# Kernel tuning notes

Hardware: AMD Instinct MI355X
Metric: run time of the kernel (lower is better)

The kernel has to match this reference:

```python
import jax, jax.numpy as jnp
import numpy as np

D_MODEL = 1024
NUM_HEADS = 16
HEAD_DIM = D_MODEL // NUM_HEADS


def setup_inputs() -> dict:
    key = jax.random.key(0)
    ks = jax.random.split(key, 9)
    s = 1.0 / np.sqrt(D_MODEL)
    def lin(k):
        kw, kb = jax.random.split(k)
        W = jax.random.uniform(kw, (D_MODEL, D_MODEL), jnp.float32, -s, s)
        b = jax.random.uniform(kb, (D_MODEL,), jnp.float32, -s, s)
        return W, b
    Wq, bq = lin(ks[0])
    Wk, bk = lin(ks[1])
    Wv, bv = lin(ks[2])
    Wo, bo = lin(ks[3])
    x = jax.random.normal(ks[4], (4, 2048, D_MODEL), jnp.float32)
    return {"x": x, "Wq": Wq, "bq": bq, "Wk": Wk, "bk": bk,
            "Wv": Wv, "bv": bv, "Wo": Wo, "bo": bo}


def reference(x, Wq, bq, Wk, bk, Wv, bv, Wo, bo):
    B, S, _ = x.shape
    def heads(W, b):
        # [B,S,D] -> [B,H,S,Dh]
        return (x @ W.T + b).reshape(B, S, NUM_HEADS, HEAD_DIM).transpose(0, 2, 1, 3)
    q = heads(Wq, bq)
    k = heads(Wk, bk)
    v = heads(Wv, bv)
    scale = jnp.sqrt(jnp.float32(HEAD_DIM))
    scores = jnp.einsum('bhqd,bhkd->bhqk', q, k) / scale  # [B,H,S,S]
    attn = jax.nn.softmax(scores, axis=-1)
    ctx = jnp.einsum('bhqk,bhkd->bhqd', attn, v)
    ctx = ctx.transpose(0, 2, 1, 3).reshape(B, S, D_MODEL)
    out = ctx @ Wo.T + bo
    return out
```

## Files before the change

kernel.cpp:

```cpp
#include <hip/hip_runtime.h>
#include <hip/hip_bf16.h>

typedef __bf16 bf16;
typedef __attribute__((ext_vector_type(4))) __bf16 bf16x4;
typedef __attribute__((ext_vector_type(8))) __bf16 bf16x8;
typedef __attribute__((ext_vector_type(4))) float floatx4;

#define MFMA_16x16x32(a, b, c) __builtin_amdgcn_mfma_f32_16x16x32_bf16((a), (b), (c), 0, 0, 0)

__device__ __forceinline__ void async_lds16(const bf16* g, bf16* lds) {
  __builtin_amdgcn_global_load_lds(
      (__attribute__((address_space(1))) void*)(g),
      (__attribute__((address_space(3))) void*)(lds),
      16, 0, 0);
}

__global__ __launch_bounds__(256) void cast_kernel(const float* __restrict__ src,
                                                   bf16* __restrict__ dst, int n) {
  int i = (blockIdx.x * 256 + threadIdx.x) * 8;
  if (i >= n) return;
  floatx4 a = *(const floatx4*)(src + i);
  floatx4 b = *(const floatx4*)(src + i + 4);
  bf16x8 r;
  r[0] = (bf16)a[0]; r[1] = (bf16)a[1]; r[2] = (bf16)a[2]; r[3] = (bf16)a[3];
  r[4] = (bf16)b[0]; r[5] = (bf16)b[1]; r[6] = (bf16)b[2]; r[7] = (bf16)b[3];
  *(bf16x8*)(dst + i) = r;
}

template <typename CT, bool VT>
__device__ __forceinline__ void gemm_async_body(
    const bf16* __restrict__ A, const bf16* __restrict__ W,
    const float* __restrict__ bias, CT* __restrict__ C)
{
  __shared__ __align__(16) bf16 As[128 * 64];
  __shared__ __align__(16) bf16 Bs[128 * 64];

  const int tid  = threadIdx.x;
  const int lane = tid & 63;
  const int wave = tid >> 6;
  const int quad = lane >> 4;
  const int l15  = lane & 15;

  const int gm0   = blockIdx.y * 128;
  const int gn0   = blockIdx.x * 128;
  const int m_off = (wave >> 1) * 64;
  const int n_off = (wave & 1) * 64;

  floatx4 acc[4][4] = {};

  const bf16* ap[4];
  const bf16* wp[4];
  #pragma unroll
  for (int i = 0; i < 4; ++i) {
    int c = i * 256 + tid;
    int srow = c >> 3;
    int ksw  = (c & 7) ^ (srow & 7);
    ap[i] = A + (size_t)(gm0 + srow) * 1024 + ksw * 8;
    wp[i] = W + (size_t)(gn0 + srow) * 1024 + ksw * 8;
  }

  for (int kt = 0; kt < 16; ++kt) {
    __syncthreads();
    #pragma unroll
    for (int i = 0; i < 4; ++i) {
      int c = i * 256 + tid;
      async_lds16(ap[i], &As[c * 8]);
      async_lds16(wp[i], &Bs[c * 8]);
      ap[i] += 64; wp[i] += 64;
    }
    __syncthreads();

    #pragma unroll
    for (int kk = 0; kk < 2; ++kk) {
      bf16x8 af[4], bfr[4];
      #pragma unroll
      for (int i = 0; i < 4; ++i) {
        int rm = m_off + i * 16 + l15;
        af[i]  = *(const bf16x8*)&As[rm * 64 + (((kk * 4 + quad) ^ (rm & 7)) * 8)];
        int rn = n_off + i * 16 + l15;
        bfr[i] = *(const bf16x8*)&Bs[rn * 64 + (((kk * 4 + quad) ^ (rn & 7)) * 8)];
      }
      #pragma unroll
      for (int i = 0; i < 4; ++i)
        #pragma unroll
        for (int j = 0; j < 4; ++j)
          acc[i][j] = MFMA_16x16x32(af[i], bfr[j], acc[i][j]);
    }
  }

  #pragma unroll
  for (int j = 0; j < 4; ++j) {
    const int gcol = gn0 + n_off + j * 16 + l15;
    const float bv = bias[gcol];
    #pragma unroll
    for (int i = 0; i < 4; ++i) {
      const int gr = gm0 + m_off + i * 16 + quad * 4;
      if constexpr (VT) {
        const int h  = gcol >> 6;
        const int dh = gcol & 63;
        const size_t base =
            (((size_t)(gr >> 11) * 16 + h) * 64 + dh) * 2048 + (gr & 2047);
        bf16x4 pk;
        #pragma unroll
        for (int r = 0; r < 4; ++r) pk[r] = (bf16)(acc[i][j][r] + bv);
        *(bf16x4*)&C[base] = pk;
      } else {
        #pragma unroll
        for (int r = 0; r < 4; ++r)
          C[(size_t)(gr + r) * 1024 + gcol] = (CT)(acc[i][j][r] + bv);
      }
    }
  }
}

__global__ __launch_bounds__(256) void qk_gemm_async(
    const bf16* __restrict__ xb,
    const bf16* __restrict__ Wqb, const float* __restrict__ bq,
    const bf16* __restrict__ Wkb, const float* __restrict__ bk,
    bf16* Q, bf16* K)
{
  const bf16* W = blockIdx.z ? Wkb : Wqb;
  const float* bias = blockIdx.z ? bk : bq;
  bf16* out = blockIdx.z ? K : Q;
  gemm_async_body<bf16, false>(xb, W, bias, out);
}

__global__ __launch_bounds__(256) void v_gemm_async(
    const bf16* __restrict__ xb, const bf16* __restrict__ Wvb,
    const float* __restrict__ bv, bf16* __restrict__ Vt)
{
  gemm_async_body<bf16, true>(xb, Wvb, bv, Vt);
}

__global__ __launch_bounds__(256) void o_gemm_async(
    const bf16* __restrict__ ctx, const bf16* __restrict__ Wob,
    const float* __restrict__ bo, float* __restrict__ out)
{
  gemm_async_body<float, false>(ctx, Wob, bo, out);
}

__global__ __launch_bounds__(512) void flash3_kernel(
    const bf16* __restrict__ Q, const bf16* __restrict__ Kg,
    const bf16* __restrict__ Vtg, bf16* __restrict__ ctx)
{
  __shared__ __align__(16) bf16 Ks[64 * 64];
  __shared__ __align__(16) bf16 Vts[64 * 64];
  __shared__ __align__(16) bf16 Ps[8 * 16 * 72];

  const int tid  = threadIdx.x;
  const int lane = tid & 63;
  const int wave = tid >> 6;
  const int quad = lane >> 4;
  const int l15  = lane & 15;

  const int bh = blockIdx.y;
  const int b  = bh >> 4;
  const int h  = bh & 15;
  const int qt = blockIdx.x;

  const size_t row0 = (size_t)b * 2048;
  const int col0 = h * 64;

  const int qs = qt * 128 + wave * 16 + l15;
  const bf16* qp = Q + (row0 + qs) * 1024 + col0 + quad * 8;
  const bf16x8 qf0 = *(const bf16x8*)(qp);
  const bf16x8 qf1 = *(const bf16x8*)(qp + 32);

  floatx4 o_acc[4] = {};
  float l_part[4] = {0.0f, 0.0f, 0.0f, 0.0f};
  const float SC = 0.125f * 1.44269504088896341f;

  const int srow = tid >> 3;
  const int ksw  = (tid & 7) ^ (srow & 7);
  const bf16* kp = Kg + (row0 + srow) * 1024 + col0 + ksw * 8;
  const bf16* vp = Vtg + ((size_t)bh * 64 + srow) * 2048 + ksw * 8;
  bf16* const ksd = &Ks[tid * 8];
  bf16* const vtd = &Vts[tid * 8];

  for (int kb = 0; kb < 32; ++kb) {
    __syncthreads();
    async_lds16(kp, ksd);
    async_lds16(vp, vtd);
    kp += 64 * 1024;
    vp += 64;
    __syncthreads();

    floatx4 sc[4];
    #pragma unroll
    for (int j = 0; j < 4; ++j) {
      int rk = j * 16 + l15;
      bf16x8 k0 = *(const bf16x8*)&Ks[rk * 64 + ((quad ^ (rk & 7)) * 8)];
      bf16x8 k1 = *(const bf16x8*)&Ks[rk * 64 + (((4 + quad) ^ (rk & 7)) * 8)];
      floatx4 z = {};
      z = MFMA_16x16x32(qf0, k0, z);
      z = MFMA_16x16x32(qf1, k1, z);
      sc[j] = z;
    }

    #pragma unroll
    for (int j = 0; j < 4; ++j)
      #pragma unroll
      for (int r = 0; r < 4; ++r) {
        float p = exp2f(fminf(sc[j][r] * SC, 60.0f));
        sc[j][r] = p;
        l_part[r] += p;
      }

    #pragma unroll
    for (int j = 0; j < 4; ++j)
      #pragma unroll
      for (int r = 0; r < 4; ++r)
        Ps[(wave * 16 + quad * 4 + r) * 72 + j * 16 + l15] = (bf16)sc[j][r];

    #pragma unroll
    for (int kk = 0; kk < 2; ++kk) {
      bf16x8 pf = *(const bf16x8*)&Ps[(wave * 16 + l15) * 72 + kk * 32 + quad * 8];
      #pragma unroll
      for (int t = 0; t < 4; ++t) {
        int rd = t * 16 + l15;
        bf16x8 vf = *(const bf16x8*)&Vts[rd * 64 + (((kk * 4 + quad) ^ (rd & 7)) * 8)];
        o_acc[t] = MFMA_16x16x32(pf, vf, o_acc[t]);
      }
    }
  }

  #pragma unroll
  for (int off = 1; off < 16; off <<= 1)
    #pragma unroll
    for (int r = 0; r < 4; ++r)
      l_part[r] += __shfl_xor(l_part[r], off, 64);
  #pragma unroll
  for (int r = 0; r < 4; ++r) l_part[r] = 1.0f / l_part[r];

  #pragma unroll
  for (int t = 0; t < 4; ++t)
    #pragma unroll
    for (int r = 0; r < 4; ++r) {
      int srow2 = qt * 128 + wave * 16 + quad * 4 + r;
      ctx[(row0 + srow2) * 1024 + col0 + t * 16 + l15] = (bf16)(o_acc[t][r] * l_part[r]);
    }
}

__device__ __forceinline__ bf16x8 load8(const bf16* p) { return *(const bf16x8*)p; }
__device__ __forceinline__ bf16x8 load8(const float* p) {
  floatx4 a = *(const floatx4*)p;
  floatx4 b = *(const floatx4*)(p + 4);
  bf16x8 r;
  r[0] = (bf16)a[0]; r[1] = (bf16)a[1]; r[2] = (bf16)a[2]; r[3] = (bf16)a[3];
  r[4] = (bf16)b[0]; r[5] = (bf16)b[1]; r[6] = (bf16)b[2]; r[7] = (bf16)b[3];
  return r;
}

template <typename AT, typename CT>
__device__ __forceinline__ void gemm128_body_fb(
    const AT* __restrict__ A, const float* __restrict__ W,
    const float* __restrict__ bias, CT* __restrict__ C)
{
  constexpr int LDP = 72;
  __shared__ __align__(16) bf16 As[128 * LDP];
  __shared__ __align__(16) bf16 Bs[128 * LDP];
  const int tid = threadIdx.x, lane = tid & 63, wave = tid >> 6;
  const int quad = lane >> 4, l15 = lane & 15;
  const int gm0 = blockIdx.y * 128, gn0 = blockIdx.x * 128;
  const int m_off = (wave >> 1) * 64, n_off = (wave & 1) * 64;
  floatx4 acc[4][4] = {};
  int srow[4], scol[4];
  #pragma unroll
  for (int i = 0; i < 4; ++i) {
    int c = i * 256 + tid;
    srow[i] = c >> 3; scol[i] = (c & 7) * 8;
  }
  for (int kt = 0; kt < 16; ++kt) {
    bf16x8 ar[4], br[4];
    #pragma unroll
    for (int i = 0; i < 4; ++i) {
      ar[i] = load8(A + (size_t)(gm0 + srow[i]) * 1024 + kt * 64 + scol[i]);
      br[i] = load8(W + (size_t)(gn0 + srow[i]) * 1024 + kt * 64 + scol[i]);
    }
    __syncthreads();
    #pragma unroll
    for (int i = 0; i < 4; ++i) {
      *(bf16x8*)&As[srow[i] * LDP + scol[i]] = ar[i];
      *(bf16x8*)&Bs[srow[i] * LDP + scol[i]] = br[i];
    }
    __syncthreads();
    #pragma unroll
    for (int kk = 0; kk < 2; ++kk) {
      bf16x8 af[4], bfr[4];
      #pragma unroll
      for (int i = 0; i < 4; ++i) {
        af[i]  = *(const bf16x8*)&As[(m_off + i * 16 + l15) * LDP + (kk * 4 + quad) * 8];
        bfr[i] = *(const bf16x8*)&Bs[(n_off + i * 16 + l15) * LDP + (kk * 4 + quad) * 8];
      }
      #pragma unroll
      for (int i = 0; i < 4; ++i)
        #pragma unroll
        for (int j = 0; j < 4; ++j)
          acc[i][j] = MFMA_16x16x32(af[i], bfr[j], acc[i][j]);
    }
  }
  #pragma unroll
  for (int j = 0; j < 4; ++j) {
    const int gcol = gn0 + n_off + j * 16 + l15;
    const float bv = bias[gcol];
    #pragma unroll
    for (int i = 0; i < 4; ++i) {
      const int gr = gm0 + m_off + i * 16 + quad * 4;
      #pragma unroll
      for (int r = 0; r < 4; ++r)
        C[(size_t)(gr + r) * 1024 + gcol] = (CT)(acc[i][j][r] + bv);
    }
  }
}

__global__ __launch_bounds__(256) void qkv_gemm_fb(
    const float* __restrict__ x,
    const float* __restrict__ Wq, const float* __restrict__ bq,
    const float* __restrict__ Wk, const float* __restrict__ bk,
    const float* __restrict__ Wv, const float* __restrict__ bv,
    bf16* Q, bf16* K, bf16* V)
{
  const float* W; const float* bias; bf16* out;
  if (blockIdx.z == 0)      { W = Wq; bias = bq; out = Q; }
  else if (blockIdx.z == 1) { W = Wk; bias = bk; out = K; }
  else                      { W = Wv; bias = bv; out = V; }
  gemm128_body_fb<float, bf16>(x, W, bias, out);
}

__global__ __launch_bounds__(256) void out_gemm_fb(
    const bf16* __restrict__ ctx, const float* __restrict__ Wo,
    const float* __restrict__ bo, float* __restrict__ out)
{
  gemm128_body_fb<bf16, float>(ctx, Wo, bo, out);
}

__global__ __launch_bounds__(512) void flash_fb(
    const bf16* Q, const bf16* __restrict__ Kg, const bf16* __restrict__ Vg,
    bf16* ctx)
{
  __shared__ __align__(16) bf16 Ks[64 * 72];
  __shared__ __align__(16) bf16 Vs[64 * 72];
  __shared__ __align__(16) bf16 Vt[64 * 72];
  __shared__ __align__(16) bf16 Ps[8 * 16 * 72];
  const int tid = threadIdx.x, lane = tid & 63, wave = tid >> 6;
  const int quad = lane >> 4, l15 = lane & 15;
  const int bh = blockIdx.y, b = bh >> 4, h = bh & 15, qt = blockIdx.x;
  const size_t row0 = (size_t)b * 2048;
  const int col0 = h * 64;
  const int qs = qt * 128 + wave * 16 + l15;
  const bf16* qp = Q + (row0 + qs) * 1024 + col0 + quad * 8;
  const bf16x8 qf0 = *(const bf16x8*)(qp);
  const bf16x8 qf1 = *(const bf16x8*)(qp + 32);
  floatx4 o_acc[4] = {};
  float l_part[4] = {0.0f, 0.0f, 0.0f, 0.0f};
  const float SC = 0.125f * 1.44269504088896341f;
  const int srow = tid >> 3, scol = (tid & 7) * 8;
  const bf16* kptr = Kg + (row0 + srow) * 1024 + col0 + scol;
  const bf16* vptr = Vg + (row0 + srow) * 1024 + col0 + scol;
  const int td = tid & 63, tg = tid >> 6;
  for (int kb = 0; kb < 32; ++kb) {
    bf16x8 kr = *(const bf16x8*)kptr;
    bf16x8 vr = *(const bf16x8*)vptr;
    kptr += 64 * 1024; vptr += 64 * 1024;
    __syncthreads();
    *(bf16x8*)&Ks[srow * 72 + scol] = kr;
    *(bf16x8*)&Vs[srow * 72 + scol] = vr;
    __syncthreads();
    {
      bf16x8 t;
      #pragma unroll
      for (int j = 0; j < 8; ++j) t[j] = Vs[(tg * 8 + j) * 72 + td];
      *(bf16x8*)&Vt[td * 72 + tg * 8] = t;
    }
    floatx4 sc[4];
    #pragma unroll
    for (int j = 0; j < 4; ++j) {
      int rk = j * 16 + l15;
      bf16x8 k0 = *(const bf16x8*)&Ks[rk * 72 + quad * 8];
      bf16x8 k1 = *(const bf16x8*)&Ks[rk * 72 + 32 + quad * 8];
      floatx4 z = {};
      z = MFMA_16x16x32(qf0, k0, z);
      z = MFMA_16x16x32(qf1, k1, z);
      sc[j] = z;
    }
    #pragma unroll
    for (int j = 0; j < 4; ++j)
      #pragma unroll
      for (int r = 0; r < 4; ++r) {
        float p = exp2f(fminf(sc[j][r] * SC, 60.0f));
        sc[j][r] = p;
        l_part[r] += p;
      }
    #pragma unroll
    for (int j = 0; j < 4; ++j)
      #pragma unroll
      for (int r = 0; r < 4; ++r)
        Ps[(wave * 16 + quad * 4 + r) * 72 + j * 16 + l15] = (bf16)sc[j][r];
    __syncthreads();
    #pragma unroll
    for (int kk = 0; kk < 2; ++kk) {
      bf16x8 pf = *(const bf16x8*)&Ps[(wave * 16 + l15) * 72 + kk * 32 + quad * 8];
      #pragma unroll
      for (int t = 0; t < 4; ++t) {
        bf16x8 vf = *(const bf16x8*)&Vt[(t * 16 + l15) * 72 + kk * 32 + quad * 8];
        o_acc[t] = MFMA_16x16x32(pf, vf, o_acc[t]);
      }
    }
  }
  #pragma unroll
  for (int off = 1; off < 16; off <<= 1)
    #pragma unroll
    for (int r = 0; r < 4; ++r)
      l_part[r] += __shfl_xor(l_part[r], off, 64);
  #pragma unroll
  for (int r = 0; r < 4; ++r) l_part[r] = 1.0f / l_part[r];
  #pragma unroll
  for (int t = 0; t < 4; ++t)
    #pragma unroll
    for (int r = 0; r < 4; ++r) {
      int srow2 = qt * 128 + wave * 16 + quad * 4 + r;
      ctx[(row0 + srow2) * 1024 + col0 + t * 16 + l15] = (bf16)(o_acc[t][r] * l_part[r]);
    }
}

extern "C" void kernel_launch(void* const* d_in, const int* in_sizes, int n_in,
                              void* d_out, int out_size, void* d_ws, size_t ws_size,
                              hipStream_t stream) {
  (void)in_sizes; (void)n_in; (void)out_size;
  const float* x  = (const float*)d_in[0];
  const float* Wq = (const float*)d_in[1];
  const float* bq = (const float*)d_in[2];
  const float* Wk = (const float*)d_in[3];
  const float* bk = (const float*)d_in[4];
  const float* Wv = (const float*)d_in[5];
  const float* bv = (const float*)d_in[6];
  const float* Wo = (const float*)d_in[7];
  const float* bo = (const float*)d_in[8];
  float* out = (float*)d_out;

  const size_t nE = (size_t)8192 * 1024;
  const size_t wE = (size_t)1024 * 1024;
  const size_t need = (5 * nE + 4 * wE) * sizeof(bf16);

  if (ws_size >= need) {
    bf16* Qw   = (bf16*)d_ws;
    bf16* Kw   = Qw + nE;
    bf16* Vtw  = Kw + nE;
    bf16* ctxw = Vtw + nE;
    bf16* xb   = ctxw + nE;
    bf16* Wqb  = xb + nE;
    bf16* Wkb  = Wqb + wE;
    bf16* Wvb  = Wkb + wE;
    bf16* Wob  = Wvb + wE;

    cast_kernel<<<dim3(4096), 256, 0, stream>>>(x, xb, (int)nE);
    cast_kernel<<<dim3(512), 256, 0, stream>>>(Wq, Wqb, (int)wE);
    cast_kernel<<<dim3(512), 256, 0, stream>>>(Wk, Wkb, (int)wE);
    cast_kernel<<<dim3(512), 256, 0, stream>>>(Wv, Wvb, (int)wE);
    cast_kernel<<<dim3(512), 256, 0, stream>>>(Wo, Wob, (int)wE);

    qk_gemm_async<<<dim3(8, 64, 2), 256, 0, stream>>>(xb, Wqb, bq, Wkb, bk, Qw, Kw);
    v_gemm_async<<<dim3(8, 64), 256, 0, stream>>>(xb, Wvb, bv, Vtw);
    flash3_kernel<<<dim3(16, 64), 512, 0, stream>>>(Qw, Kw, Vtw, ctxw);
    o_gemm_async<<<dim3(8, 64), 256, 0, stream>>>(ctxw, Wob, bo, out);
  } else {
    bf16* Qw = (bf16*)d_ws;
    bf16* Kw = Qw + nE;
    bf16* Vw = Kw + nE;
    bf16* ctx = (ws_size >= 4 * nE * sizeof(bf16)) ? (Vw + nE) : Qw;
    qkv_gemm_fb<<<dim3(8, 64, 3), 256, 0, stream>>>(x, Wq, bq, Wk, bk, Wv, bv, Qw, Kw, Vw);
    flash_fb<<<dim3(16, 64), 512, 0, stream>>>(Qw, Kw, Vw, ctx);
    out_gemm_fb<<<dim3(8, 64), 256, 0, stream>>>(ctx, Wo, bo, out);
  }
}
```

Measured before the change: 338.5 us.

## Fuse QKV projection launch, fold softmax scale into Q, double flash KV tile

Combines the Q/K and V projection GEMMs into one launch with a z-dimension of three. The softmax scale is applied to Q in the GEMM epilogue, so the flash kernel skips a multiply per score. The flash kernel now processes 128 keys per iteration instead of 64, halving the loop trips and barriers. In exchange, LDS usage roughly doubles, which may reduce occupancy, and Q picks up a slight rounding change.

```diff
diff --git a/kernel.cpp b/kernel.cpp
--- a/kernel.cpp
+++ b/kernel.cpp
@@ -7,6 +7,8 @@
 typedef __attribute__((ext_vector_type(4))) float floatx4;
 
 #define MFMA_16x16x32(a, b, c) __builtin_amdgcn_mfma_f32_16x16x32_bf16((a), (b), (c), 0, 0, 0)
+
+#define SOFTMAX_SC 0.18033688011112042f
 
 __device__ __forceinline__ void async_lds16(const bf16* g, bf16* lds) {
   __builtin_amdgcn_global_load_lds(
@@ -30,7 +32,7 @@
 template <typename CT, bool VT>
 __device__ __forceinline__ void gemm_async_body(
     const bf16* __restrict__ A, const bf16* __restrict__ W,
-    const float* __restrict__ bias, CT* __restrict__ C)
+    const float* __restrict__ bias, CT* __restrict__ C, float oscale)
 {
   __shared__ __align__(16) bf16 As[128 * 64];
   __shared__ __align__(16) bf16 Bs[128 * 64];
@@ -107,45 +109,41 @@
       } else {
         #pragma unroll
         for (int r = 0; r < 4; ++r)
-          C[(size_t)(gr + r) * 1024 + gcol] = (CT)(acc[i][j][r] + bv);
-      }
-    }
-  }
-}
-
-__global__ __launch_bounds__(256) void qk_gemm_async(
+          C[(size_t)(gr + r) * 1024 + gcol] = (CT)((acc[i][j][r] + bv) * oscale);
+      }
+    }
+  }
+}
+
+__global__ __launch_bounds__(256) void qkv_gemm_async(
     const bf16* __restrict__ xb,
     const bf16* __restrict__ Wqb, const float* __restrict__ bq,
     const bf16* __restrict__ Wkb, const float* __restrict__ bk,
-    bf16* Q, bf16* K)
-{
-  const bf16* W = blockIdx.z ? Wkb : Wqb;
-  const float* bias = blockIdx.z ? bk : bq;
-  bf16* out = blockIdx.z ? K : Q;
-  gemm_async_body<bf16, false>(xb, W, bias, out);
-}
-
-__global__ __launch_bounds__(256) void v_gemm_async(
-    const bf16* __restrict__ xb, const bf16* __restrict__ Wvb,
-    const float* __restrict__ bv, bf16* __restrict__ Vt)
-{
-  gemm_async_body<bf16, true>(xb, Wvb, bv, Vt);
+    const bf16* __restrict__ Wvb, const float* __restrict__ bv,
+    bf16* Q, bf16* K, bf16* Vt)
+{
+  if (blockIdx.z == 0)
+    gemm_async_body<bf16, false>(xb, Wqb, bq, Q, SOFTMAX_SC);
+  else if (blockIdx.z == 1)
+    gemm_async_body<bf16, false>(xb, Wkb, bk, K, 1.0f);
+  else
+    gemm_async_body<bf16, true>(xb, Wvb, bv, Vt, 1.0f);
 }
 
 __global__ __launch_bounds__(256) void o_gemm_async(
     const bf16* __restrict__ ctx, const bf16* __restrict__ Wob,
     const float* __restrict__ bo, float* __restrict__ out)
 {
-  gemm_async_body<float, false>(ctx, Wob, bo, out);
-}
-
-__global__ __launch_bounds__(512) void flash3_kernel(
+  gemm_async_body<float, false>(ctx, Wob, bo, out, 1.0f);
+}
+
+__global__ __launch_bounds__(512) void flash4_kernel(
     const bf16* __restrict__ Q, const bf16* __restrict__ Kg,
     const bf16* __restrict__ Vtg, bf16* __restrict__ ctx)
 {
-  __shared__ __align__(16) bf16 Ks[64 * 64];
-  __shared__ __align__(16) bf16 Vts[64 * 64];
-  __shared__ __align__(16) bf16 Ps[8 * 16 * 72];
+  __shared__ __align__(16) bf16 Ks[128 * 64];
+  __shared__ __align__(16) bf16 Vts[64 * 128];
+  __shared__ __align__(16) bf16 Ps[8 * 16 * 136];
 
   const int tid  = threadIdx.x;
   const int lane = tid & 63;
@@ -168,26 +166,34 @@
 
   floatx4 o_acc[4] = {};
   float l_part[4] = {0.0f, 0.0f, 0.0f, 0.0f};
-  const float SC = 0.125f * 1.44269504088896341f;
-
-  const int srow = tid >> 3;
-  const int ksw  = (tid & 7) ^ (srow & 7);
-  const bf16* kp = Kg + (row0 + srow) * 1024 + col0 + ksw * 8;
-  const bf16* vp = Vtg + ((size_t)bh * 64 + srow) * 2048 + ksw * 8;
-  bf16* const ksd = &Ks[tid * 8];
-  bf16* const vtd = &Vts[tid * 8];
-
-  for (int kb = 0; kb < 32; ++kb) {
-    __syncthreads();
-    async_lds16(kp, ksd);
-    async_lds16(vp, vtd);
-    kp += 64 * 1024;
-    vp += 64;
-    __syncthreads();
-
-    floatx4 sc[4];
-    #pragma unroll
-    for (int j = 0; j < 4; ++j) {
+
+  const int krow0 = tid >> 3;
+  const int kksw0 = (tid & 7) ^ (krow0 & 7);
+  const int krow1 = (tid + 512) >> 3;
+  const int kksw1 = (tid & 7) ^ (krow1 & 7);
+  const int vd0   = tid >> 4;
+  const int vsw0  = (tid & 15) ^ (vd0 & 7);
+  const int vd1   = (tid + 512) >> 4;
+  const int vsw1  = (tid & 15) ^ (vd1 & 7);
+
+  const bf16* kp0 = Kg + (row0 + krow0) * 1024 + col0 + kksw0 * 8;
+  const bf16* kp1 = Kg + (row0 + krow1) * 1024 + col0 + kksw1 * 8;
+  const bf16* vp0 = Vtg + ((size_t)bh * 64 + vd0) * 2048 + vsw0 * 8;
+  const bf16* vp1 = Vtg + ((size_t)bh * 64 + vd1) * 2048 + vsw1 * 8;
+
+  for (int kb = 0; kb < 16; ++kb) {
+    __syncthreads();
+    async_lds16(kp0, &Ks[tid * 8]);
+    async_lds16(kp1, &Ks[(tid + 512) * 8]);
+    async_lds16(vp0, &Vts[tid * 8]);
+    async_lds16(vp1, &Vts[(tid + 512) * 8]);
+    kp0 += 128 * 1024; kp1 += 128 * 1024;
+    vp0 += 128;        vp1 += 128;
+    __syncthreads();
+
+    floatx4 sc[8];
+    #pragma unroll
+    for (int j = 0; j < 8; ++j) {
       int rk = j * 16 + l15;
       bf16x8 k0 = *(const bf16x8*)&Ks[rk * 64 + ((quad ^ (rk & 7)) * 8)];
       bf16x8 k1 = *(const bf16x8*)&Ks[rk * 64 + (((4 + quad) ^ (rk & 7)) * 8)];
@@ -198,27 +204,27 @@
     }
 
     #pragma unroll
-    for (int j = 0; j < 4; ++j)
+    for (int j = 0; j < 8; ++j)
       #pragma unroll
       for (int r = 0; r < 4; ++r) {
-        float p = exp2f(fminf(sc[j][r] * SC, 60.0f));
+        float p = exp2f(fminf(sc[j][r], 60.0f));
         sc[j][r] = p;
         l_part[r] += p;
       }
 
     #pragma unroll
-    for (int j = 0; j < 4; ++j)
+    for (int j = 0; j < 8; ++j)
       #pragma unroll
       for (int r = 0; r < 4; ++r)
-        Ps[(wave * 16 + quad * 4 + r) * 72 + j * 16 + l15] = (bf16)sc[j][r];
-
-    #pragma unroll
-    for (int kk = 0; kk < 2; ++kk) {
-      bf16x8 pf = *(const bf16x8*)&Ps[(wave * 16 + l15) * 72 + kk * 32 + quad * 8];
+        Ps[(wave * 16 + quad * 4 + r) * 136 + j * 16 + l15] = (bf16)sc[j][r];
+
+    #pragma unroll
+    for (int kk = 0; kk < 4; ++kk) {
+      bf16x8 pf = *(const bf16x8*)&Ps[(wave * 16 + l15) * 136 + kk * 32 + quad * 8];
       #pragma unroll
       for (int t = 0; t < 4; ++t) {
         int rd = t * 16 + l15;
-        bf16x8 vf = *(const bf16x8*)&Vts[rd * 64 + (((kk * 4 + quad) ^ (rd & 7)) * 8)];
+        bf16x8 vf = *(const bf16x8*)&Vts[rd * 128 + (((kk * 4 + quad) ^ (rd & 7)) * 8)];
         o_acc[t] = MFMA_16x16x32(pf, vf, o_acc[t]);
       }
     }
@@ -353,7 +359,7 @@
   const bf16x8 qf1 = *(const bf16x8*)(qp + 32);
   floatx4 o_acc[4] = {};
   float l_part[4] = {0.0f, 0.0f, 0.0f, 0.0f};
-  const float SC = 0.125f * 1.44269504088896341f;
+  const float SC = SOFTMAX_SC;
   const int srow = tid >> 3, scol = (tid & 7) * 8;
   const bf16* kptr = Kg + (row0 + srow) * 1024 + col0 + scol;
   const bf16* vptr = Vg + (row0 + srow) * 1024 + col0 + scol;
@@ -459,9 +465,9 @@
     cast_kernel<<<dim3(512), 256, 0, stream>>>(Wv, Wvb, (int)wE);
     cast_kernel<<<dim3(512), 256, 0, stream>>>(Wo, Wob, (int)wE);
 
-    qk_gemm_async<<<dim3(8, 64, 2), 256, 0, stream>>>(xb, Wqb, bq, Wkb, bk, Qw, Kw);
-    v_gemm_async<<<dim3(8, 64), 256, 0, stream>>>(xb, Wvb, bv, Vtw);
-    flash3_kernel<<<dim3(16, 64), 512, 0, stream>>>(Qw, Kw, Vtw, ctxw);
+    qkv_gemm_async<<<dim3(8, 64, 3), 256, 0, stream>>>(
+        xb, Wqb, bq, Wkb, bk, Wvb, bv, Qw, Kw, Vtw);
+    flash4_kernel<<<dim3(16, 64), 512, 0, stream>>>(Qw, Kw, Vtw, ctxw);
     o_gemm_async<<<dim3(8, 64), 256, 0, stream>>>(ctxw, Wob, bo, out);
   } else {
     bf16* Qw = (bf16*)d_ws;
```

Measured after the change: 374.5 us. 10.7% more time.

## Fuse Q/K/V projections into one 256-row-tile GEMM and fold softmax scale into Q

Applied to the files above, without the earlier changes.

Replaces the separate QK and V projection launches with a single kernel using 512 threads, 256x128 output tiles and a grid z-dimension of 3. The softmax scale times log2(e) is applied to Q when it is stored, so the attention kernel skips a multiply per score element. The aim is to cut launch count, reuse each x tile across more output columns, and shave ALU work in the softmax. Risks are extra LDS use per block (48KB) and lower precision because the scaled Q is rounded to bf16.

```diff
diff --git a/kernel.cpp b/kernel.cpp
--- a/kernel.cpp
+++ b/kernel.cpp
@@ -7,6 +7,8 @@
 typedef __attribute__((ext_vector_type(4))) float floatx4;
 
 #define MFMA_16x16x32(a, b, c) __builtin_amdgcn_mfma_f32_16x16x32_bf16((a), (b), (c), 0, 0, 0)
+
+#define SOFTMAX_SC 0.18033688011112042f
 
 __device__ __forceinline__ void async_lds16(const bf16* g, bf16* lds) {
   __builtin_amdgcn_global_load_lds(
@@ -27,8 +29,8 @@
   *(bf16x8*)(dst + i) = r;
 }
 
-template <typename CT, bool VT>
-__device__ __forceinline__ void gemm_async_body(
+template <typename CT>
+__device__ __forceinline__ void gemm128_async_body(
     const bf16* __restrict__ A, const bf16* __restrict__ W,
     const float* __restrict__ bias, CT* __restrict__ C)
 {
@@ -95,7 +97,104 @@
     #pragma unroll
     for (int i = 0; i < 4; ++i) {
       const int gr = gm0 + m_off + i * 16 + quad * 4;
-      if constexpr (VT) {
+      #pragma unroll
+      for (int r = 0; r < 4; ++r)
+        C[(size_t)(gr + r) * 1024 + gcol] = (CT)(acc[i][j][r] + bv);
+    }
+  }
+}
+
+__global__ __launch_bounds__(256) void o_gemm_async(
+    const bf16* __restrict__ ctx, const bf16* __restrict__ Wob,
+    const float* __restrict__ bo, float* __restrict__ out)
+{
+  gemm128_async_body<float>(ctx, Wob, bo, out);
+}
+
+__global__ __launch_bounds__(512, 4) void qkv_gemm256(
+    const bf16* __restrict__ xb,
+    const bf16* __restrict__ Wqb, const float* __restrict__ bq,
+    const bf16* __restrict__ Wkb, const float* __restrict__ bk,
+    const bf16* __restrict__ Wvb, const float* __restrict__ bv,
+    bf16* Q, bf16* K, bf16* Vt)
+{
+  __shared__ __align__(16) bf16 As[256 * 64];
+  __shared__ __align__(16) bf16 Bs[128 * 64];
+
+  const int z = blockIdx.z;
+  const bf16* W = (z == 0) ? Wqb : (z == 1) ? Wkb : Wvb;
+  const float* bias = (z == 0) ? bq : (z == 1) ? bk : bv;
+
+  const int tid  = threadIdx.x;
+  const int lane = tid & 63;
+  const int wave = tid >> 6;
+  const int quad = lane >> 4;
+  const int l15  = lane & 15;
+
+  const int gm0   = blockIdx.y * 256;
+  const int gn0   = blockIdx.x * 128;
+  const int m_off = (wave >> 1) * 64;
+  const int n_off = (wave & 1) * 64;
+
+  floatx4 acc[4][4] = {};
+
+  const bf16* ap[4];
+  const bf16* wp[2];
+  #pragma unroll
+  for (int i = 0; i < 4; ++i) {
+    int c = i * 512 + tid;
+    int srow = c >> 3;
+    int ksw  = (c & 7) ^ (srow & 7);
+    ap[i] = xb + (size_t)(gm0 + srow) * 1024 + ksw * 8;
+  }
+  #pragma unroll
+  for (int i = 0; i < 2; ++i) {
+    int c = i * 512 + tid;
+    int srow = c >> 3;
+    int ksw  = (c & 7) ^ (srow & 7);
+    wp[i] = W + (size_t)(gn0 + srow) * 1024 + ksw * 8;
+  }
+
+  for (int kt = 0; kt < 16; ++kt) {
+    __syncthreads();
+    #pragma unroll
+    for (int i = 0; i < 4; ++i) {
+      async_lds16(ap[i], &As[(i * 512 + tid) * 8]);
+      ap[i] += 64;
+    }
+    #pragma unroll
+    for (int i = 0; i < 2; ++i) {
+      async_lds16(wp[i], &Bs[(i * 512 + tid) * 8]);
+      wp[i] += 64;
+    }
+    __syncthreads();
+
+    #pragma unroll
+    for (int kk = 0; kk < 2; ++kk) {
+      bf16x8 af[4], bfr[4];
+      #pragma unroll
+      for (int i = 0; i < 4; ++i) {
+        int rm = m_off + i * 16 + l15;
+        af[i]  = *(const bf16x8*)&As[rm * 64 + (((kk * 4 + quad) ^ (rm & 7)) * 8)];
+        int rn = n_off + i * 16 + l15;
+        bfr[i] = *(const bf16x8*)&Bs[rn * 64 + (((kk * 4 + quad) ^ (rn & 7)) * 8)];
+      }
+      #pragma unroll
+      for (int i = 0; i < 4; ++i)
+        #pragma unroll
+        for (int j = 0; j < 4; ++j)
+          acc[i][j] = MFMA_16x16x32(af[i], bfr[j], acc[i][j]);
+    }
+  }
+
+  #pragma unroll
+  for (int j = 0; j < 4; ++j) {
+    const int gcol = gn0 + n_off + j * 16 + l15;
+    const float bv = bias[gcol];
+    #pragma unroll
+    for (int i = 0; i < 4; ++i) {
+      const int gr = gm0 + m_off + i * 16 + quad * 4;
+      if (z == 2) {
         const int h  = gcol >> 6;
         const int dh = gcol & 63;
         const size_t base =
@@ -103,43 +202,19 @@
         bf16x4 pk;
         #pragma unroll
         for (int r = 0; r < 4; ++r) pk[r] = (bf16)(acc[i][j][r] + bv);
-        *(bf16x4*)&C[base] = pk;
+        *(bf16x4*)&Vt[base] = pk;
       } else {
+        bf16* dst = (z == 0) ? Q : K;
+        const float sc = (z == 0) ? SOFTMAX_SC : 1.0f;
         #pragma unroll
         for (int r = 0; r < 4; ++r)
-          C[(size_t)(gr + r) * 1024 + gcol] = (CT)(acc[i][j][r] + bv);
-      }
-    }
-  }
-}
-
-__global__ __launch_bounds__(256) void qk_gemm_async(
-    const bf16* __restrict__ xb,
-    const bf16* __restrict__ Wqb, const float* __restrict__ bq,
-    const bf16* __restrict__ Wkb, const float* __restrict__ bk,
-    bf16* Q, bf16* K)
-{
-  const bf16* W = blockIdx.z ? Wkb : Wqb;
-  const float* bias = blockIdx.z ? bk : bq;
-  bf16* out = blockIdx.z ? K : Q;
-  gemm_async_body<bf16, false>(xb, W, bias, out);
-}
-
-__global__ __launch_bounds__(256) void v_gemm_async(
-    const bf16* __restrict__ xb, const bf16* __restrict__ Wvb,
-    const float* __restrict__ bv, bf16* __restrict__ Vt)
-{
-  gemm_async_body<bf16, true>(xb, Wvb, bv, Vt);
-}
-
-__global__ __launch_bounds__(256) void o_gemm_async(
-    const bf16* __restrict__ ctx, const bf16* __restrict__ Wob,
-    const float* __restrict__ bo, float* __restrict__ out)
-{
-  gemm_async_body<float, false>(ctx, Wob, bo, out);
-}
-
-__global__ __launch_bounds__(512) void flash3_kernel(
+          dst[(size_t)(gr + r) * 1024 + gcol] = (bf16)((acc[i][j][r] + bv) * sc);
+      }
+    }
+  }
+}
+
+__global__ __launch_bounds__(512) void flash3b_kernel(
     const bf16* __restrict__ Q, const bf16* __restrict__ Kg,
     const bf16* __restrict__ Vtg, bf16* __restrict__ ctx)
 {
@@ -168,7 +243,6 @@
 
   floatx4 o_acc[4] = {};
   float l_part[4] = {0.0f, 0.0f, 0.0f, 0.0f};
-  const float SC = 0.125f * 1.44269504088896341f;
 
   const int srow = tid >> 3;
   const int ksw  = (tid & 7) ^ (srow & 7);
@@ -201,7 +275,7 @@
     for (int j = 0; j < 4; ++j)
       #pragma unroll
       for (int r = 0; r < 4; ++r) {
-        float p = exp2f(fminf(sc[j][r] * SC, 60.0f));
+        float p = exp2f(fminf(sc[j][r], 60.0f));
         sc[j][r] = p;
         l_part[r] += p;
       }
@@ -353,7 +427,7 @@
   const bf16x8 qf1 = *(const bf16x8*)(qp + 32);
   floatx4 o_acc[4] = {};
   float l_part[4] = {0.0f, 0.0f, 0.0f, 0.0f};
-  const float SC = 0.125f * 1.44269504088896341f;
+  const float SC = SOFTMAX_SC;
   const int srow = tid >> 3, scol = (tid & 7) * 8;
   const bf16* kptr = Kg + (row0 + srow) * 1024 + col0 + scol;
   const bf16* vptr = Vg + (row0 + srow) * 1024 + col0 + scol;
@@ -459,9 +533,9 @@
     cast_kernel<<<dim3(512), 256, 0, stream>>>(Wv, Wvb, (int)wE);
     cast_kernel<<<dim3(512), 256, 0, stream>>>(Wo, Wob, (int)wE);
 
-    qk_gemm_async<<<dim3(8, 64, 2), 256, 0, stream>>>(xb, Wqb, bq, Wkb, bk, Qw, Kw);
-    v_gemm_async<<<dim3(8, 64), 256, 0, stream>>>(xb, Wvb, bv, Vtw);
-    flash3_kernel<<<dim3(16, 64), 512, 0, stream>>>(Qw, Kw, Vtw, ctxw);
+    qkv_gemm256<<<dim3(8, 32, 3), 512, 0, stream>>>(
+        xb, Wqb, bq, Wkb, bk, Wvb, bv, Qw, Kw, Vtw);
+    flash3b_kernel<<<dim3(16, 64), 512, 0, stream>>>(Qw, Kw, Vtw, ctxw);
     o_gemm_async<<<dim3(8, 64), 256, 0, stream>>>(ctxw, Wob, bo, out);
   } else {
     bf16* Qw = (bf16*)d_ws;
```

New measurement: 332.1 us. No clear change (-1.9%).
